# Kernel optimization log

Measured on AMD Instinct MI355X. Metric: run time of the kernel, lower is better.

## Reference

```python
import jax, jax.numpy as jnp
import numpy as np

CHANNELS = 32


def _mlp(x, W1, b1, W2, b2, W3, b3):
    # FNN: Linear -> ReLU -> Linear -> ReLU -> Linear (last layer linear)
    h = jax.nn.relu(x @ W1 + b1)
    h = jax.nn.relu(h @ W2 + b2)
    return h @ W3 + b3


def setup_inputs() -> dict:
    key = jax.random.key(0)
    ks = jax.random.split(key, 8)
    E = 262144
    C = CHANNELS
    H = 128
    d_in = 4  # 2 * spatial_dim
    d_out = C * (C + 1)  # 1056
    s = lambda fan_in: 1.0 / np.sqrt(fan_in)
    return {
        "pos_i": jax.random.normal(ks[0], (E, 2), jnp.float32),
        "pos_j": jax.random.normal(ks[1], (E, 2), jnp.float32),
        "v_j": jax.random.normal(ks[2], (E, C), jnp.float32),
        "W1": jax.random.normal(ks[3], (d_in, H), jnp.float32) * s(d_in),
        "b1": jnp.zeros((H,), jnp.float32),
        "W2": jax.random.normal(ks[4], (H, H), jnp.float32) * s(H),
        "b2": jnp.zeros((H,), jnp.float32),
        "W3": jax.random.normal(ks[5], (H, d_out), jnp.float32) * s(H),
        "b3": jnp.zeros((d_out,), jnp.float32),
    }


def reference(pos_i, pos_j, v_j, W1, b1, W2, b2, W3, b3):
    C = CHANNELS
    pos_ij = jnp.concatenate((pos_i, pos_j), axis=-1)          # [E, 2*spatial_dim]
    kernel = _mlp(pos_ij, W1, b1, W2, b2, W3, b3)
    kernel = kernel.reshape(-1, C, C + 1)                      # [E, C, C+1]
    mat, bias = kernel[..., :, :-1], kernel[..., :, -1]        # [E,C,C], [E,C]
    return jnp.einsum('eij,ej->ei', mat, v_j) + bias           # [E, C]
```

## Files before the change

### kernel.cpp

```cpp
#include <hip/hip_runtime.h>


#define E_TOTAL 262144
#define EPB 256
#define NBLK (E_TOTAL / EPB)

typedef float f32x4 __attribute__((ext_vector_type(4)));
typedef short s8v  __attribute__((ext_vector_type(8)));

__device__ __forceinline__ unsigned short f2bf(float x) {
  unsigned u = __float_as_uint(x);
  u += 0x7fffu + ((u >> 16) & 1u);
  return (unsigned short)(u >> 16);
}

__global__ void prep_pack(const float* __restrict__ W2, const float* __restrict__ W3,
                          const float* __restrict__ b3,
                          unsigned short* __restrict__ Wg2, unsigned short* __restrict__ W2f,
                          unsigned short* __restrict__ b3f, float* __restrict__ b3c) {
  int idx = blockIdx.x * 256 + threadIdx.x;
  if (idx < 135168) {
    int jj = idx & 7, lane = (idx >> 3) & 63;
    int ksnn = idx >> 9, ks = ksnn & 3, nn = ksnn >> 2;
    int nnt = (nn < 33) ? (2 * nn) : (2 * (nn - 33) + 1);
    int k = ks * 32 + ((lane >> 4) << 3) + jj;
    int col = nnt * 16 + (lane & 15);
    int i = col & 31, j = col >> 5;
    Wg2[idx] = f2bf(W3[k * 1056 + i * 33 + j]);
  }
  if (idx < 16384) {
    int ks = idx >> 12, nt = (idx >> 9) & 7, l = (idx >> 3) & 63, jj = idx & 7;
    int k = ks * 32 + ((l >> 4) << 3) + jj;
    int n = nt * 16 + (l & 15);
    W2f[idx] = f2bf(W2[k * 128 + n]);
  }
  if (idx < 1024) {
    int jj = idx & 7, lane = (idx >> 3) & 63, ih = idx >> 9;
    int j = ((lane >> 4) << 3) + jj, i = ih * 16 + (lane & 15);
    b3f[idx] = f2bf(b3[i * 33 + j]);
  }
  if (idx < 32) b3c[idx] = b3[idx * 33 + 32];
}

template <int IH>
__device__ __forceinline__ void g_tile(const s8v (&bfr)[4], const float* __restrict__ vt,
                                       int j, int eoff,
                                       const s8v (&af)[4][4], float (&oa)[2][4][4]) {
  const f32x4 zero4 = {0.f, 0.f, 0.f, 0.f};
  f32x4 p[4];
#pragma unroll
  for (int m = 0; m < 4; ++m)
    p[m] = __builtin_amdgcn_mfma_f32_16x16x32_bf16(af[m][0], bfr[0], zero4, 0, 0, 0);
#pragma unroll
  for (int ks = 1; ks < 4; ++ks)
#pragma unroll
    for (int m = 0; m < 4; ++m)
      p[m] = __builtin_amdgcn_mfma_f32_16x16x32_bf16(af[m][ks], bfr[ks], p[m], 0, 0, 0);
  const float* vp = vt + j * 260 + eoff;
#pragma unroll
  for (int m = 0; m < 4; ++m) {
    f32x4 vv = *(const f32x4*)(vp + m * 16);
#pragma unroll
    for (int r = 0; r < 4; ++r) oa[IH][m][r] += vv[r] * p[m][r];
  }
}

template <int IH>
__device__ __forceinline__ void g_pass(const unsigned short* __restrict__ Wg2,
                                       const float* __restrict__ vt,
                                       int lane, int eoff,
                                       const s8v (&af)[4][4], float (&oa)[2][4][4]) {
  const unsigned short* base = Wg2 + IH * 33 * 2048 + lane * 8;
  s8v bnx[4];
#pragma unroll
  for (int ks = 0; ks < 4; ++ks) bnx[ks] = *(const s8v*)(base + ks * 512);
  for (int j = 0; j < 32; ++j) {
    s8v bfr[4];
#pragma unroll
    for (int ks = 0; ks < 4; ++ks) bfr[ks] = bnx[ks];
#pragma unroll
    for (int ks = 0; ks < 4; ++ks)
      bnx[ks] = *(const s8v*)(base + (j + 1) * 2048 + ks * 512);
    g_tile<IH>(bfr, vt, j, eoff, af, oa);
  }
  g_tile<IH>(bnx, vt, 32, eoff, af, oa);
}

__global__ __launch_bounds__(256, 2) void fnn_fused(
    const float* __restrict__ pos_i, const float* __restrict__ pos_j,
    const float* __restrict__ vj, const float* __restrict__ W1,
    const float* __restrict__ b1, const float* __restrict__ b2,
    const unsigned short* __restrict__ W2f, const unsigned short* __restrict__ Wg2,
    const unsigned short* __restrict__ b3f, const float* __restrict__ b3c,
    float* __restrict__ out) {
  __shared__ __attribute__((aligned(16))) char smem[36864];
  float* vt = (float*)smem;
  unsigned short* h1c = (unsigned short*)smem;
  unsigned short* h2n = (unsigned short*)(smem + 18432);

  const int tid = threadIdx.x;
  const int w = tid >> 6, lane = tid & 63, q = lane >> 4, ln = lane & 15;
  const int B0 = blockIdx.x * EPB;
  const int eoff = w * 64 + q * 4;

  float oa[2][4][4];
  {
    s8v av[4];
#pragma unroll
    for (int m = 0; m < 4; ++m) {
      int e = B0 + w * 64 + m * 16 + ln;
      const float4 va = *(const float4*)(vj + (size_t)e * 32 + q * 8);
      const float4 vb = *(const float4*)(vj + (size_t)e * 32 + q * 8 + 4);
      s8v t;
      t[0] = (short)f2bf(va.x); t[1] = (short)f2bf(va.y);
      t[2] = (short)f2bf(va.z); t[3] = (short)f2bf(va.w);
      t[4] = (short)f2bf(vb.x); t[5] = (short)f2bf(vb.y);
      t[6] = (short)f2bf(vb.z); t[7] = (short)f2bf(vb.w);
      av[m] = t;
    }
#pragma unroll
    for (int ih = 0; ih < 2; ++ih) {
      s8v b3fr = *(const s8v*)(b3f + (ih * 64 + lane) * 8);
      float cbv = b3c[ih * 16 + ln];
      f32x4 ci = {cbv, cbv, cbv, cbv};
#pragma unroll
      for (int m = 0; m < 4; ++m) {
        f32x4 p = __builtin_amdgcn_mfma_f32_16x16x32_bf16(av[m], b3fr, ci, 0, 0, 0);
#pragma unroll
        for (int r = 0; r < 4; ++r) oa[ih][m][r] = p[r];
      }
    }
  }

  const int hh0 = (tid & 15) * 8;
  float w1r[4][8], b1r[8], b2r[8];
#pragma unroll
  for (int d = 0; d < 4; ++d)
#pragma unroll
    for (int u = 0; u < 8; ++u) w1r[d][u] = W1[d * 128 + hh0 + u];
#pragma unroll
  for (int u = 0; u < 8; ++u) b1r[u] = b1[hh0 + u];
#pragma unroll
  for (int nt = 0; nt < 8; ++nt) b2r[nt] = b2[nt * 16 + ln];

  s8v af[4][4];
  for (int qtr = 0; qtr < 4; ++qtr) {
#pragma unroll
    for (int half = 0; half < 4; ++half) {
      int ee = (tid >> 4) + half * 16;
      int eg = B0 + qtr * 64 + ee;
      float2 pi = *(const float2*)(pos_i + (size_t)eg * 2);
      float2 pj = *(const float2*)(pos_j + (size_t)eg * 2);
      s8v hv;
#pragma unroll
      for (int u = 0; u < 8; ++u) {
        float o = b1r[u] + pi.x * w1r[0][u] + pi.y * w1r[1][u] +
                  pj.x * w1r[2][u] + pj.y * w1r[3][u];
        hv[u] = (short)f2bf(fmaxf(o, 0.f));
      }
      *(s8v*)&h1c[ee * 144 + hh0] = hv;
    }
    __syncthreads();
    {
      s8v afr[4];
#pragma unroll
      for (int ks = 0; ks < 4; ++ks)
        afr[ks] = *(const s8v*)&h1c[(w * 16 + ln) * 144 + ks * 32 + q * 8];
#pragma unroll
      for (int nt = 0; nt < 8; ++nt) {
        f32x4 a4 = {0.f, 0.f, 0.f, 0.f};
#pragma unroll
        for (int ks = 0; ks < 4; ++ks) {
          s8v bfr2 = *(const s8v*)(W2f + ((ks * 8 + nt) * 64 + lane) * 8);
          a4 = __builtin_amdgcn_mfma_f32_16x16x32_bf16(afr[ks], bfr2, a4, 0, 0, 0);
        }
#pragma unroll
        for (int r = 0; r < 4; ++r)
          h2n[(w * 16 + q * 4 + r) * 144 + nt * 16 + ln] =
              f2bf(fmaxf(a4[r] + b2r[nt], 0.f));
      }
    }
    __syncthreads();
    if (w == qtr) {
#pragma unroll
      for (int m = 0; m < 4; ++m)
#pragma unroll
        for (int ks = 0; ks < 4; ++ks)
          af[m][ks] = *(const s8v*)&h2n[(m * 16 + ln) * 144 + ks * 32 + q * 8];
    }
  }
  __syncthreads();

  {
    const float* vrow = vj + (size_t)(B0 + tid) * 32;
#pragma unroll
    for (int j4 = 0; j4 < 8; ++j4) {
      float4 vv = *(const float4*)(vrow + j4 * 4);
      vt[(j4 * 4 + 0) * 260 + tid] = vv.x;
      vt[(j4 * 4 + 1) * 260 + tid] = vv.y;
      vt[(j4 * 4 + 2) * 260 + tid] = vv.z;
      vt[(j4 * 4 + 3) * 260 + tid] = vv.w;
    }
    vt[32 * 260 + tid] = 1.0f;
  }
  __syncthreads();

  g_pass<0>(Wg2, vt, lane, eoff, af, oa);
  g_pass<1>(Wg2, vt, lane, eoff, af, oa);

#pragma unroll
  for (int m = 0; m < 4; ++m)
#pragma unroll
    for (int ih = 0; ih < 2; ++ih)
#pragma unroll
      for (int r = 0; r < 4; ++r) {
        int e = B0 + w * 64 + m * 16 + q * 4 + r;
        out[(size_t)e * 32 + ih * 16 + ln] = oa[ih][m][r];
      }
}

extern "C" void kernel_launch(void* const* d_in, const int* in_sizes, int n_in,
                              void* d_out, int out_size, void* d_ws, size_t ws_size,
                              hipStream_t stream) {
  const float* pos_i = (const float*)d_in[0];
  const float* pos_j = (const float*)d_in[1];
  const float* vj    = (const float*)d_in[2];
  const float* W1    = (const float*)d_in[3];
  const float* b1    = (const float*)d_in[4];
  const float* W2    = (const float*)d_in[5];
  const float* b2    = (const float*)d_in[6];
  const float* W3    = (const float*)d_in[7];
  const float* b3    = (const float*)d_in[8];
  float* outp = (float*)d_out;

  unsigned short* Wg2 = (unsigned short*)d_ws;
  unsigned short* W2f = (unsigned short*)((char*)d_ws + 270336);
  unsigned short* b3f = (unsigned short*)((char*)d_ws + 303104);
  float*          b3c = (float*)((char*)d_ws + 305152);

  prep_pack<<<528, 256, 0, stream>>>(W2, W3, b3, Wg2, W2f, b3f, b3c);
  fnn_fused<<<NBLK, 256, 0, stream>>>(pos_i, pos_j, vj, W1, b1, b2, W2f, Wg2, b3f, b3c, outp);
}
```

Before: 220.4 us.

## Stage W3 fragments through LDS with double-buffered async global_load_lds

Instead of each wave loading its W3 B-fragments straight from global memory into registers, the block cooperatively streams 3-tile chunks of packed W3 into a double-buffered LDS region using global_load_lds, with one barrier per chunk. This removes redundant per-wave global traffic for the same weights and overlaps the next chunk's fetch with the current chunk's MFMA work. The vt padding drops from 260 to 256 floats per row, which may bring LDS bank conflicts back. LDS use grows to about 57 KB per block, which could limit occupancy, and the 22 per-chunk barriers add synchronisation cost.

```diff
diff --git a/kernel.cpp b/kernel.cpp
--- a/kernel.cpp
+++ b/kernel.cpp
@@ -12,6 +12,12 @@
   unsigned u = __float_as_uint(x);
   u += 0x7fffu + ((u >> 16) & 1u);
   return (unsigned short)(u >> 16);
+}
+
+__device__ __forceinline__ void gld16(const void* g, void* l) {
+  __builtin_amdgcn_global_load_lds(
+      (const __attribute__((address_space(1))) unsigned int*)g,
+      (__attribute__((address_space(3))) unsigned int*)l, 16, 0, 0);
 }
 
 __global__ void prep_pack(const float* __restrict__ W2, const float* __restrict__ W3,
@@ -43,47 +49,34 @@
 }
 
 template <int IH>
-__device__ __forceinline__ void g_tile(const s8v (&bfr)[4], const float* __restrict__ vt,
-                                       int j, int eoff,
-                                       const s8v (&af)[4][4], float (&oa)[2][4][4]) {
+__device__ __forceinline__ void g_chunk(const unsigned short* __restrict__ buf,
+                                        const float* __restrict__ vt,
+                                        int j0, int lane, int eoff,
+                                        const s8v (&af)[4][4], float (&oa)[2][4][4]) {
   const f32x4 zero4 = {0.f, 0.f, 0.f, 0.f};
-  f32x4 p[4];
-#pragma unroll
-  for (int m = 0; m < 4; ++m)
-    p[m] = __builtin_amdgcn_mfma_f32_16x16x32_bf16(af[m][0], bfr[0], zero4, 0, 0, 0);
-#pragma unroll
-  for (int ks = 1; ks < 4; ++ks)
+#pragma unroll
+  for (int t = 0; t < 3; ++t) {
+    s8v bfr[4];
+#pragma unroll
+    for (int ks = 0; ks < 4; ++ks)
+      bfr[ks] = *(const s8v*)&buf[t * 2048 + ks * 512 + lane * 8];
+    f32x4 p[4];
 #pragma unroll
     for (int m = 0; m < 4; ++m)
-      p[m] = __builtin_amdgcn_mfma_f32_16x16x32_bf16(af[m][ks], bfr[ks], p[m], 0, 0, 0);
-  const float* vp = vt + j * 260 + eoff;
-#pragma unroll
-  for (int m = 0; m < 4; ++m) {
-    f32x4 vv = *(const f32x4*)(vp + m * 16);
-#pragma unroll
-    for (int r = 0; r < 4; ++r) oa[IH][m][r] += vv[r] * p[m][r];
-  }
-}
-
-template <int IH>
-__device__ __forceinline__ void g_pass(const unsigned short* __restrict__ Wg2,
-                                       const float* __restrict__ vt,
-                                       int lane, int eoff,
-                                       const s8v (&af)[4][4], float (&oa)[2][4][4]) {
-  const unsigned short* base = Wg2 + IH * 33 * 2048 + lane * 8;
-  s8v bnx[4];
-#pragma unroll
-  for (int ks = 0; ks < 4; ++ks) bnx[ks] = *(const s8v*)(base + ks * 512);
-  for (int j = 0; j < 32; ++j) {
-    s8v bfr[4];
-#pragma unroll
-    for (int ks = 0; ks < 4; ++ks) bfr[ks] = bnx[ks];
-#pragma unroll
-    for (int ks = 0; ks < 4; ++ks)
-      bnx[ks] = *(const s8v*)(base + (j + 1) * 2048 + ks * 512);
-    g_tile<IH>(bfr, vt, j, eoff, af, oa);
-  }
-  g_tile<IH>(bnx, vt, 32, eoff, af, oa);
+      p[m] = __builtin_amdgcn_mfma_f32_16x16x32_bf16(af[m][0], bfr[0], zero4, 0, 0, 0);
+#pragma unroll
+    for (int ks = 1; ks < 4; ++ks)
+#pragma unroll
+      for (int m = 0; m < 4; ++m)
+        p[m] = __builtin_amdgcn_mfma_f32_16x16x32_bf16(af[m][ks], bfr[ks], p[m], 0, 0, 0);
+    const float* vp = vt + (j0 + t) * 256 + eoff;
+#pragma unroll
+    for (int m = 0; m < 4; ++m) {
+      f32x4 vv = *(const f32x4*)(vp + m * 16);
+#pragma unroll
+      for (int r = 0; r < 4; ++r) oa[IH][m][r] += vv[r] * p[m][r];
+    }
+  }
 }
 
 __global__ __launch_bounds__(256, 2) void fnn_fused(
@@ -93,8 +86,9 @@
     const unsigned short* __restrict__ W2f, const unsigned short* __restrict__ Wg2,
     const unsigned short* __restrict__ b3f, const float* __restrict__ b3c,
     float* __restrict__ out) {
-  __shared__ __attribute__((aligned(16))) char smem[36864];
+  __shared__ __attribute__((aligned(16))) char smem[58368];
   float* vt = (float*)smem;
+  unsigned short* Bb  = (unsigned short*)(smem + 33792);
   unsigned short* h1c = (unsigned short*)smem;
   unsigned short* h2n = (unsigned short*)(smem + 18432);
 
@@ -196,17 +190,34 @@
 #pragma unroll
     for (int j4 = 0; j4 < 8; ++j4) {
       float4 vv = *(const float4*)(vrow + j4 * 4);
-      vt[(j4 * 4 + 0) * 260 + tid] = vv.x;
-      vt[(j4 * 4 + 1) * 260 + tid] = vv.y;
-      vt[(j4 * 4 + 2) * 260 + tid] = vv.z;
-      vt[(j4 * 4 + 3) * 260 + tid] = vv.w;
-    }
-    vt[32 * 260 + tid] = 1.0f;
+      vt[(j4 * 4 + 0) * 256 + tid] = vv.x;
+      vt[(j4 * 4 + 1) * 256 + tid] = vv.y;
+      vt[(j4 * 4 + 2) * 256 + tid] = vv.z;
+      vt[(j4 * 4 + 3) * 256 + tid] = vv.w;
+    }
+    vt[32 * 256 + tid] = 1.0f;
+  }
+
+  {
+    const char* g = (const char*)Wg2 + tid * 16;
+    char* l = (char*)Bb + (tid & 192) * 16;
+#pragma unroll
+    for (int t = 0; t < 3; ++t) gld16(g + t * 4096, l + t * 4096);
   }
   __syncthreads();
 
-  g_pass<0>(Wg2, vt, lane, eoff, af, oa);
-  g_pass<1>(Wg2, vt, lane, eoff, af, oa);
+  for (int c = 0; c < 22; ++c) {
+    const unsigned short* buf = Bb + (c & 1) * 6144;
+    if (c + 1 < 22) {
+      const char* g = (const char*)Wg2 + (c + 1) * 12288 + tid * 16;
+      char* l = (char*)Bb + ((c + 1) & 1) * 12288 + (tid & 192) * 16;
+#pragma unroll
+      for (int t = 0; t < 3; ++t) gld16(g + t * 4096, l + t * 4096);
+    }
+    if (c < 11) g_chunk<0>(buf, vt, c * 3, lane, eoff, af, oa);
+    else        g_chunk<1>(buf, vt, (c - 11) * 3, lane, eoff, af, oa);
+    __syncthreads();
+  }
 
 #pragma unroll
   for (int m = 0; m < 4; ++m)
```

New measurement: 218.9 us. No clear change (-0.7%).
